# Performance work log

Measured on AMD Instinct MI355X. Metric: run time of the kernel, lower is better.

## Reference

```python
import jax, jax.numpy as jnp
import numpy as np

D_MODEL = 1024
N_HEADS = 16
FACTOR = 2
KEY_DIM = D_MODEL // N_HEADS            # 64
HEAD_DIM = D_MODEL * FACTOR // N_HEADS  # 128
SCALING = KEY_DIM ** -0.5
BSZ, SEQ = 2, 2048


def _rel_pos(slen):
    # angle: 1/10000**linspace(0,1,key_dim//2), each value repeated twice
    half = jnp.asarray(1.0) / jnp.power(10000.0, jnp.linspace(0.0, 1.0, KEY_DIM // 2))
    angle = jnp.repeat(half, 2)                              # [key_dim]
    decay = jnp.log(1.0 - 2.0 ** (-5.0 - jnp.arange(N_HEADS, dtype=jnp.float32)))  # [h], negative
    idx = jnp.arange(slen, dtype=jnp.float32)
    sin = jnp.sin(idx[:, None] * angle[None, :])             # [s, key_dim]
    cos = jnp.cos(idx[:, None] * angle[None, :])
    diff = idx[:, None] - idx[None, :]                       # [s, s]
    tril = diff >= 0
    mask = jnp.where(tril[None], jnp.exp(diff[None] * decay[:, None, None]), 0.0)  # [h, s, s]
    mask = mask / jnp.sqrt(mask.sum(axis=-1, keepdims=True))
    return sin, cos, mask


def _rotate_every_two(x):
    x1 = x[..., ::2]
    x2 = x[..., 1::2]
    return jnp.stack((-x2, x1), axis=-1).reshape(x.shape)


def _theta_shift(x, sin, cos):
    return x * cos + _rotate_every_two(x) * sin


def setup_inputs() -> dict:
    key = jax.random.key(0)
    ks = jax.random.split(key, 11)
    s = 1.0 / np.sqrt(D_MODEL)
    s2 = 1.0 / np.sqrt(D_MODEL * FACTOR)
    return {
        "x": jax.random.normal(ks[0], (BSZ, SEQ, D_MODEL), jnp.float32),
        "q_w": jax.random.uniform(ks[1], (D_MODEL, D_MODEL), jnp.float32, -s, s),
        "q_b": jax.random.uniform(ks[2], (D_MODEL,), jnp.float32, -s, s),
        "k_w": jax.random.uniform(ks[3], (D_MODEL, D_MODEL), jnp.float32, -s, s),
        "k_b": jax.random.uniform(ks[4], (D_MODEL,), jnp.float32, -s, s),
        "v_w": jax.random.uniform(ks[5], (D_MODEL, D_MODEL * FACTOR), jnp.float32, -s, s),
        "v_b": jax.random.uniform(ks[6], (D_MODEL * FACTOR,), jnp.float32, -s, s),
        "g_w": jax.random.uniform(ks[7], (D_MODEL, D_MODEL * FACTOR), jnp.float32, -s, s),
        "g_b": jax.random.uniform(ks[8], (D_MODEL * FACTOR,), jnp.float32, -s, s),
        "o_w": jax.random.uniform(ks[9], (D_MODEL * FACTOR, D_MODEL), jnp.float32, -s2, s2),
        "o_b": jax.random.uniform(ks[10], (D_MODEL,), jnp.float32, -s2, s2),
    }


def _forward(x, q_w, q_b, k_w, k_b, v_w, v_b, g_w, g_b, o_w, o_b):
    bsz, slen, _ = x.shape
    sin, cos, mask = _rel_pos(slen)
    q = x @ q_w + q_b
    k = (x @ k_w + k_b) * SCALING
    v = x @ v_w + v_b
    g = x @ g_w + g_b
    # [b, h, s, key_dim]
    q = q.reshape(bsz, slen, N_HEADS, KEY_DIM).transpose(0, 2, 1, 3)
    k = k.reshape(bsz, slen, N_HEADS, KEY_DIM).transpose(0, 2, 1, 3)
    qr = _theta_shift(q, sin, cos)
    kr = _theta_shift(k, sin, cos)
    vr = v.reshape(bsz, slen, N_HEADS, HEAD_DIM).transpose(0, 2, 1, 3)  # [b,h,s,head_dim]
    qk = jnp.einsum('bhmd,bhnd->bhmn', qr, kr) * mask                  # decay-masked scores
    denom = jnp.clip(jnp.abs(jax.lax.stop_gradient(qk).sum(axis=-1, keepdims=True)), 1.0, None)
    qk = qk / denom
    out = jnp.einsum('bhmn,bhnd->bhmd', qk, vr).transpose(0, 2, 1, 3)  # [b,s,h,head_dim]
    # per-head LayerNorm over head_dim, no affine
    mu = out.mean(axis=-1, keepdims=True)
    var = out.var(axis=-1, keepdims=True)
    out = (out - mu) / jnp.sqrt(var + 1e-5)
    out = out.reshape(bsz, slen, N_HEADS * HEAD_DIM)
    out = jax.nn.silu(g) * out
    return out @ o_w + o_b


def reference(x, q_w, q_b, k_w, k_b, v_w, v_b, g_w, g_b, o_w, o_b):
    return _forward(x, q_w, q_b, k_w, k_b, v_w, v_b, g_w, g_b, o_w, o_b)
```

## Files before the change

### kernel.cpp

```cpp
#include <hip/hip_runtime.h>
#include <hip/hip_bf16.h>


typedef __hip_bfloat16 bf16;
typedef short bf16x4 __attribute__((ext_vector_type(4)));
typedef short bf16x8 __attribute__((ext_vector_type(8)));
typedef float floatx4 __attribute__((ext_vector_type(4)));

#define B_SZ 2
#define SEQ 2048
#define NH 16
#define KD 64
#define HD 128

#define ASYNC16(gp, lp)                                                             \
  __builtin_amdgcn_global_load_lds(                                                 \
      (const __attribute__((address_space(1))) unsigned int*)(unsigned long long)(const void*)(gp), \
      (__attribute__((address_space(3))) unsigned int*)(unsigned int)(unsigned long long)(void*)(lp), \
      16, 0, 0)

__device__ __forceinline__ float b2f(bf16 x) { return __bfloat162float(x); }
__device__ __forceinline__ bf16 f2b(float x) { return __float2bfloat16(x); }

#define MFMA16(a, bb, c) __builtin_amdgcn_mfma_f32_16x16x32_bf16(a, bb, c, 0, 0, 0)

__global__ void convert_k(const float* __restrict__ in, bf16* __restrict__ out) {
  int i = blockIdx.x * 256 + threadIdx.x;
  float4 v = reinterpret_cast<const float4*>(in)[i];
  union { bf16 h[4]; bf16x4 v4; } u;
  u.h[0] = f2b(v.x); u.h[1] = f2b(v.y); u.h[2] = f2b(v.z); u.h[3] = f2b(v.w);
  reinterpret_cast<bf16x4*>(out)[i] = u.v4;
}

__global__ void transpose_k(const float* __restrict__ in, bf16* __restrict__ out,
                            int K, int N) {
  __shared__ float tile[32][33];
  int tx = threadIdx.x, ty = threadIdx.y;
  int n0 = blockIdx.x * 32, k0 = blockIdx.y * 32;
#pragma unroll
  for (int j = 0; j < 4; ++j)
    tile[ty + j * 8][tx] = in[(size_t)(k0 + ty + j * 8) * N + n0 + tx];
  __syncthreads();
#pragma unroll
  for (int j = 0; j < 4; ++j)
    out[(size_t)(n0 + ty + j * 8) * K + k0 + tx] = f2b(tile[tx][ty + j * 8]);
}

template <int BM, int BN, int KDIM, int MODE>
__global__ __launch_bounds__(256, 2) void gemm_bt(
    const bf16* __restrict__ A, const bf16* __restrict__ Bt, int Ndim,
    const float* __restrict__ bias_q, const float* __restrict__ bias_k,
    const float* __restrict__ bias_v, const float* __restrict__ bias_g,
    float* __restrict__ outCqk, bf16* __restrict__ out_v,
    float* __restrict__ out_g, float* __restrict__ outF) {
  __shared__ bf16 As[BM * 32];
  __shared__ bf16 Bs[BN * 32];
  const int tid = threadIdx.x;
  const int wave = tid >> 6, lane = tid & 63;
  const int quad = lane >> 4, l16 = lane & 15;
  const int m0 = blockIdx.y * BM, n0 = blockIdx.x * BN;
  constexpr int FI = BM / 32;
  constexpr int FJ = BN / 32;
  const int wm = (wave >> 1) * (BM / 2), wn = (wave & 1) * (BN / 2);

  floatx4 acc[FI][FJ] = {};

  for (int k0 = 0; k0 < KDIM; k0 += 32) {
#pragma unroll
    for (int j = 0; j < BM / 64; ++j) {
      int cbase = (j * 4 + wave) * 64;
      int c = cbase + lane;
      const bf16* g = A + (size_t)(m0 + (c >> 2)) * KDIM + k0 + (c & 3) * 8;
      ASYNC16(g, &As[cbase * 8]);
    }
#pragma unroll
    for (int j = 0; j < BN / 64; ++j) {
      int cbase = (j * 4 + wave) * 64;
      int c = cbase + lane;
      const bf16* g = Bt + (size_t)(n0 + (c >> 2)) * KDIM + k0 + (c & 3) * 8;
      ASYNC16(g, &Bs[cbase * 8]);
    }
    __syncthreads();

    bf16x8 af[FI], bfr[FJ];
#pragma unroll
    for (int i = 0; i < FI; ++i)
      af[i] = *(const bf16x8*)&As[(wm + i * 16 + l16) * 32 + quad * 8];
#pragma unroll
    for (int j = 0; j < FJ; ++j)
      bfr[j] = *(const bf16x8*)&Bs[(wn + j * 16 + l16) * 32 + quad * 8];
#pragma unroll
    for (int i = 0; i < FI; ++i)
#pragma unroll
      for (int j = 0; j < FJ; ++j)
        acc[i][j] = MFMA16(af[i], bfr[j], acc[i][j]);
    __syncthreads();
  }

#pragma unroll
  for (int i = 0; i < FI; ++i) {
#pragma unroll
    for (int j = 0; j < FJ; ++j) {
      int gn = n0 + wn + j * 16 + l16;
      if (MODE == 0 && gn >= 2048 && gn < 4096) {
        int jj = gn - 2048;
        int s0 = m0 + wm + i * 16 + quad * 4;
        union { bf16 e[4]; unsigned long long u8; } pk;
#pragma unroll
        for (int r = 0; r < 4; ++r) pk.e[r] = f2b(acc[i][j][r] + bias_v[jj]);
        int b2 = s0 >> 11, srel = s0 & 2047;
        int h2 = jj >> 7, dloc = jj & 127;
        size_t bh2 = (size_t)b2 * NH + h2;
        size_t idx = ((bh2 * 64 + (srel >> 5)) * 8 + (dloc >> 4)) * 512 +
                     (size_t)(((srel >> 3) & 3) * 16 + (dloc & 15)) * 8 +
                     (srel & 7);
        *(unsigned long long*)&out_v[idx] = pk.u8;
      } else {
#pragma unroll
        for (int r = 0; r < 4; ++r) {
          int gm = m0 + wm + i * 16 + quad * 4 + r;
          float v = acc[i][j][r];
          if (MODE == 1) {
            v += bias_q[gn];
            outF[(size_t)gm * Ndim + gn] = v;
          } else {
            if (gn < 2048) {
              bool is_k = gn >= 1024;
              int jj = is_k ? gn - 1024 : gn;
              v += is_k ? bias_k[jj] : bias_q[jj];
              if (is_k) v *= 0.125f;
              outCqk[(size_t)gm * 2048 + gn] = v;
            } else {
              int jj = gn - 4096;
              v += bias_g[jj];
              out_g[(size_t)gm * 2048 + jj] = v;
            }
          }
        }
      }
    }
  }
}

__global__ void router_k(const float* __restrict__ Cqk,
                         bf16* __restrict__ qh, bf16* __restrict__ ql,
                         bf16* __restrict__ kh, bf16* __restrict__ kl) {
  int t = blockIdx.x * 256 + threadIdx.x;
  int row = t >> 10, pc = t & 1023;
  int b = row >> 11, s = row & 2047;
  bool is_k = pc >= 512;
  int jj = (pc - (is_k ? 512 : 0)) * 2;
  int h = jj >> 6, d = jj & 63, ii = d >> 1;
  float2 v = *(const float2*)&Cqk[(size_t)row * 2048 + pc * 2];
  float half = exp2f(-(float)ii * (13.287712379549449f / 31.0f));
  float ang = (float)s * half;
  float sn = sinf(ang), cs = cosf(ang);
  float e = v.x * cs - v.y * sn;
  float o = v.y * cs + v.x * sn;
  bf16 eh = f2b(e), oh = f2b(o);
  bf16 el = f2b(e - b2f(eh)), ol = f2b(o - b2f(oh));
  size_t idx = (((size_t)b * NH + h) * SEQ + s) * KD + d;
  bf16* ph = is_k ? kh : qh;
  bf16* pl = is_k ? kl : ql;
  union { bf16 h2[2]; unsigned u; } uh, ul;
  uh.h2[0] = eh; uh.h2[1] = oh;
  ul.h2[0] = el; ul.h2[1] = ol;
  *(unsigned*)&ph[idx] = uh.u;
  *(unsigned*)&pl[idx] = ul.u;
}

__global__ __launch_bounds__(128, 2) void retention_k(
    const bf16* __restrict__ qh, const bf16* __restrict__ ql,
    const bf16* __restrict__ kh, const bf16* __restrict__ kl,
    const bf16* __restrict__ vf, const float* __restrict__ g,
    bf16* __restrict__ gated) {
  __shared__ bf16 KHs[2][32 * 64];
  __shared__ bf16 KLs[2][32 * 64];
  const int tid = threadIdx.x;
  const int wave = tid >> 6, lane = tid & 63;
  const int quad = lane >> 4, l16 = lane & 15;
  const int bid = blockIdx.x;
  const int px_raw = bid & 31;
  const int seg = bid >> 5;
  const int h = seg & 15, b = seg >> 4;
  const int px = ((seg >> 3) & 1) ? (31 - px_raw) : px_raw;
  const int bh = b * NH + h;
  const int bt_h = 63 - px;
  const int bt_l = px;
  const int m0h = bt_h * 32 + wave * 16;
  const int m0l = bt_l * 32 + wave * 16;
  const int ntiles = bt_h + 1;
  const int lt_ntiles = bt_l + 1;

  const float t = exp2f(-(float)(5 + h));
  const float lng = log1pf(-t);
  const float log2g = lng * 1.44269504088896340736f;

  float rfh, rfl;
  {
    int mh = m0h + l16, ml = m0l + l16;
    rfh = exp2f((float)mh * log2g) *
          rsqrtf(-expm1f((float)(mh + 1) * lng) / t);
    rfl = exp2f((float)ml * log2g) *
          rsqrtf(-expm1f((float)(ml + 1) * lng) / t);
  }
  const float gstep = exp2f(-32.0f * log2g);
  float cfq[8];
#pragma unroll
  for (int i = 0; i < 8; ++i) {
    int hh = i >> 2, r = i & 3;
    cfq[i] = exp2f(-(float)(hh * 16 + quad * 4 + r) * log2g);
  }

  const size_t qoffh = ((size_t)bh * SEQ + m0h + l16) * KD;
  const size_t qoffl = ((size_t)bh * SEQ + m0l + l16) * KD;
  bf16x8 aq0h_h = *(const bf16x8*)&qh[qoffh + quad * 8];
  bf16x8 aq1h_h = *(const bf16x8*)&qh[qoffh + 32 + quad * 8];
  bf16x8 aq0l_h = *(const bf16x8*)&ql[qoffh + quad * 8];
  bf16x8 aq1l_h = *(const bf16x8*)&ql[qoffh + 32 + quad * 8];
  bf16x8 aq0h_l = *(const bf16x8*)&qh[qoffl + quad * 8];
  bf16x8 aq1h_l = *(const bf16x8*)&qh[qoffl + 32 + quad * 8];
  bf16x8 aq0l_l = *(const bf16x8*)&ql[qoffl + quad * 8];
  bf16x8 aq1l_l = *(const bf16x8*)&ql[qoffl + 32 + quad * 8];

  floatx4 oacch[8] = {}, oaccl[8] = {};
  float rsh = 0.f, rsl = 0.f;

  const bf16* khb = kh + (size_t)bh * SEQ * KD;
  const bf16* klb = kl + (size_t)bh * SEQ * KD;
  const bf16* vfb = vf + (size_t)bh * 64 * 8 * 512;
  const int lo8 = lane * 8;

  auto stage = [&](int nt, int buf) {
    const int n0s = nt * 32;
#pragma unroll
    for (int j = 0; j < 4; ++j) {
      int cc = wave * 4 + j;
      const bf16* src = (cc < 4) ? khb : klb;
      bf16* dst = (cc < 4) ? KHs[buf] : KLs[buf];
      int r = ((cc & 3) * 8) + (lane >> 3);
      int s = lane & 7;
      int q = (s - r) & 7;
      ASYNC16(src + (size_t)(n0s + r) * KD + q * 8, &dst[(cc & 3) * 512]);
    }
  };

  auto buildPA = [&](const floatx4* sc, float rf, float& rs, int n0,
                     int m0) -> bf16x8 {
    const int m = m0 + l16;
    const bool full = (m0 >= n0 + 31);
    unsigned d[4];
#pragma unroll
    for (int hh = 0; hh < 2; ++hh) {
      float p[4];
#pragma unroll
      for (int r = 0; r < 4; ++r) {
        float pv;
        if (full) {
          pv = sc[hh][r] * rf * cfq[hh * 4 + r];
        } else {
          int n = n0 + hh * 16 + quad * 4 + r;
          pv = (m >= n) ? sc[hh][r] * rf * cfq[hh * 4 + r] : 0.f;
        }
        rs += pv;
        p[r] = pv;
      }
      union { bf16 hx[2]; unsigned u; } u0, u1;
      u0.hx[0] = f2b(p[0]); u0.hx[1] = f2b(p[1]);
      u1.hx[0] = f2b(p[2]); u1.hx[1] = f2b(p[3]);
      d[hh * 2 + 0] = u0.u;
      d[hh * 2 + 1] = u1.u;
    }
    unsigned a0 = d[0], b0 = d[2];
    asm("v_permlane32_swap_b32 %0, %1" : "+v"(a0), "+v"(b0));
    asm("v_permlane16_swap_b32 %0, %1" : "+v"(a0), "+v"(b0));
    unsigned a1 = d[1], b1 = d[3];
    asm("v_permlane32_swap_b32 %0, %1" : "+v"(a1), "+v"(b1));
    asm("v_permlane16_swap_b32 %0, %1" : "+v"(a1), "+v"(b1));
    union { unsigned u[4]; bf16x8 v; } pu;
    pu.u[0] = a0; pu.u[1] = a1; pu.u[2] = b0; pu.u[3] = b1;
    return pu.v;
  };

  stage(0, 0);
  for (int nt = 0; nt < ntiles; ++nt) {
    const int n0 = nt * 32;
    const int cur = nt & 1;
    asm volatile("s_waitcnt vmcnt(0) lgkmcnt(0)" ::: "memory");
    __syncthreads();

    bf16x8 vv[8];
#pragma unroll
    for (int c = 0; c < 8; ++c)
      vv[c] = *(const bf16x8*)(vfb + ((size_t)nt * 8 + c) * 512 + lo8);

    {
      int pf = (nt + 1 < ntiles) ? nt + 1 : nt;
      stage(pf, cur ^ 1);
    }

    const bool hact = (n0 <= m0h + 15);
    const bool lact = (n0 <= m0l + 15);

    floatx4 sch[2], scl[2];
#pragma unroll
    for (int hh = 0; hh < 2; ++hh) {
      int krow = hh * 16 + l16;
      int c0 = ((quad + krow) & 7) * 8;
      int c1 = ((quad + 4 + krow) & 7) * 8;
      bf16x8 bkh0 = *(const bf16x8*)&KHs[cur][krow * 64 + c0];
      bf16x8 bkh1 = *(const bf16x8*)&KHs[cur][krow * 64 + c1];
      bf16x8 bkl0 = *(const bf16x8*)&KLs[cur][krow * 64 + c0];
      bf16x8 bkl1 = *(const bf16x8*)&KLs[cur][krow * 64 + c1];
      if (hact) {
        floatx4 z1 = {0.f, 0.f, 0.f, 0.f}, z2 = z1, z3 = z1;
        z1 = MFMA16(bkh0, aq0h_h, z1);
        z2 = MFMA16(bkh0, aq0l_h, z2);
        z3 = MFMA16(bkl0, aq0h_h, z3);
        z1 = MFMA16(bkh1, aq1h_h, z1);
        z2 = MFMA16(bkh1, aq1l_h, z2);
        z3 = MFMA16(bkl1, aq1h_h, z3);
        sch[hh] = z1 + z2 + z3;
      }
      if (lact) {
        floatx4 z1 = {0.f, 0.f, 0.f, 0.f}, z2 = z1, z3 = z1;
        z1 = MFMA16(bkh0, aq0h_l, z1);
        z2 = MFMA16(bkh0, aq0l_l, z2);
        z3 = MFMA16(bkl0, aq0h_l, z3);
        z1 = MFMA16(bkh1, aq1h_l, z1);
        z2 = MFMA16(bkh1, aq1l_l, z2);
        z3 = MFMA16(bkl1, aq1h_l, z3);
        scl[hh] = z1 + z2 + z3;
      }
    }

    bf16x8 pah, pal;
    if (hact) pah = buildPA(sch, rfh, rsh, n0, m0h);
    if (lact) pal = buildPA(scl, rfl, rsl, n0, m0l);
    rfh *= gstep;
    if (nt + 1 < lt_ntiles) rfl *= gstep;

#pragma unroll
    for (int dt = 0; dt < 8; ++dt) {
      if (hact) oacch[dt] = MFMA16(pah, vv[dt], oacch[dt]);
      if (lact) oaccl[dt] = MFMA16(pal, vv[dt], oaccl[dt]);
    }
  }

  auto finalize = [&](floatx4* oacc, float rowsum, int m0) {
    float v = rowsum;
    v += __shfl_xor(v, 16);
    v += __shfl_xor(v, 32);
    float inv_den[4];
#pragma unroll
    for (int r = 0; r < 4; ++r) {
      float dsum = __shfl(v, quad * 4 + r);
      inv_den[r] = 1.0f / fmaxf(fabsf(dsum), 1.0f);
    }
    float s1[4] = {}, s2[4] = {};
#pragma unroll
    for (int dt = 0; dt < 8; ++dt) {
#pragma unroll
      for (int r = 0; r < 4; ++r) {
        float vv2 = oacc[dt][r] * inv_den[r];
        oacc[dt][r] = vv2;
        s1[r] += vv2;
        s2[r] += vv2 * vv2;
      }
    }
    float mean[4], istd[4];
#pragma unroll
    for (int r = 0; r < 4; ++r) {
      float a = s1[r], q2 = s2[r];
      a += __shfl_xor(a, 1); a += __shfl_xor(a, 2);
      a += __shfl_xor(a, 4); a += __shfl_xor(a, 8);
      q2 += __shfl_xor(q2, 1); q2 += __shfl_xor(q2, 2);
      q2 += __shfl_xor(q2, 4); q2 += __shfl_xor(q2, 8);
      mean[r] = a * (1.0f / 128.0f);
      float var = q2 * (1.0f / 128.0f) - mean[r] * mean[r];
      istd[r] = rsqrtf(fmaxf(var, 0.0f) + 1e-5f);
    }
#pragma unroll
    for (int dt = 0; dt < 8; ++dt) {
#pragma unroll
      for (int r = 0; r < 4; ++r) {
        int m = m0 + quad * 4 + r;
        int col = h * HD + dt * 16 + l16;
        float vv2 = (oacc[dt][r] - mean[r]) * istd[r];
        float gv = g[((size_t)b * SEQ + m) * 2048 + col];
        float sg = gv / (1.0f + expf(-gv));
        gated[((size_t)b * SEQ + m) * 2048 + col] = f2b(sg * vv2);
      }
    }
  };
  finalize(oacch, rsh, m0h);
  finalize(oaccl, rsl, m0l);
}

extern "C" void kernel_launch(void* const* d_in, const int* in_sizes, int n_in,
                              void* d_out, int out_size, void* d_ws,
                              size_t ws_size, hipStream_t stream) {
  const float* x   = (const float*)d_in[0];
  const float* q_w = (const float*)d_in[1];
  const float* q_b = (const float*)d_in[2];
  const float* k_w = (const float*)d_in[3];
  const float* k_b = (const float*)d_in[4];
  const float* v_w = (const float*)d_in[5];
  const float* v_b = (const float*)d_in[6];
  const float* g_w = (const float*)d_in[7];
  const float* g_b = (const float*)d_in[8];
  const float* o_w = (const float*)d_in[9];
  const float* o_b = (const float*)d_in[10];

  char* ws = (char*)d_ws;
  bf16* Wt    = (bf16*)ws; ws += (size_t)6144 * 1024 * 2;
  bf16* oT    = (bf16*)ws; ws += (size_t)1024 * 2048 * 2;
  bf16* xb    = (bf16*)ws; ws += (size_t)4096 * 1024 * 2;
  float* Cqk  = (float*)ws; ws += (size_t)4096 * 2048 * 4;
  bf16* qhb   = (bf16*)ws; ws += (size_t)32 * 2048 * 64 * 2;
  bf16* qlb   = (bf16*)ws; ws += (size_t)32 * 2048 * 64 * 2;
  bf16* khb   = (bf16*)ws; ws += (size_t)32 * 2048 * 64 * 2;
  bf16* klb   = (bf16*)ws; ws += (size_t)32 * 2048 * 64 * 2;
  bf16* vfb   = (bf16*)ws; ws += (size_t)32 * 64 * 8 * 512 * 2;
  float* gbuf = (float*)ws; ws += (size_t)2 * 2048 * 2048 * 4;
  bf16* gated = (bf16*)ws; ws += (size_t)4096 * 2048 * 2;

  convert_k<<<(4096 * 1024 / 4) / 256, 256, 0, stream>>>(x, xb);

  dim3 tb(32, 8);
  transpose_k<<<dim3(1024 / 32, 1024 / 32), tb, 0, stream>>>(q_w, Wt, 1024, 1024);
  transpose_k<<<dim3(1024 / 32, 1024 / 32), tb, 0, stream>>>(k_w, Wt + (size_t)1024 * 1024, 1024, 1024);
  transpose_k<<<dim3(2048 / 32, 1024 / 32), tb, 0, stream>>>(v_w, Wt + (size_t)2048 * 1024, 1024, 2048);
  transpose_k<<<dim3(2048 / 32, 1024 / 32), tb, 0, stream>>>(g_w, Wt + (size_t)4096 * 1024, 1024, 2048);
  transpose_k<<<dim3(1024 / 32, 2048 / 32), tb, 0, stream>>>(o_w, oT, 2048, 1024);

  gemm_bt<128, 128, 1024, 0><<<dim3(6144 / 128, 4096 / 128), 256, 0, stream>>>(
      xb, Wt, 6144, q_b, k_b, v_b, g_b, Cqk, vfb, gbuf, nullptr);

  router_k<<<(4096 * 1024) / 256, 256, 0, stream>>>(Cqk, qhb, qlb, khb, klb);

  retention_k<<<dim3(1024), 128, 0, stream>>>(
      qhb, qlb, khb, klb, vfb, gbuf, gated);

  gemm_bt<128, 64, 2048, 1><<<dim3(1024 / 64, 4096 / 128), 256, 0, stream>>>(
      gated, oT, 1024, o_b, nullptr, nullptr, nullptr, nullptr, nullptr,
      nullptr, (float*)d_out);
}
```

Measured before the change: 333.1 us.

## Restructure retention kernel to 4 waves per contiguous 64-row block

Replaces the paired high/low row-tile scheme (two 32-row tiles per 128-thread block for load balance) with 256-thread blocks where each of four waves owns one 16-row strip of a contiguous 64-row group. The causal loop now runs over 2*grp+2 key tiles, and waves whose strip has no work skip V loads and MFMAs. This halves per-thread accumulator state, which frees registers for higher occupancy. In exchange it loses the per-block triangular load balancing, so block runtimes vary more, and the K staging cost is shared across more waves.

Result: no change. 337.1 us, median of 2 (+1.2%).

```diff
diff --git a/kernel.cpp b/kernel.cpp
--- a/kernel.cpp
+++ b/kernel.cpp
@@ -169,7 +169,7 @@
   *(unsigned*)&pl[idx] = ul.u;
 }
 
-__global__ __launch_bounds__(128, 2) void retention_k(
+__global__ __launch_bounds__(256, 4) void retention_k(
     const bf16* __restrict__ qh, const bf16* __restrict__ ql,
     const bf16* __restrict__ kh, const bf16* __restrict__ kl,
     const bf16* __restrict__ vf, const float* __restrict__ g,
@@ -180,29 +180,23 @@
   const int wave = tid >> 6, lane = tid & 63;
   const int quad = lane >> 4, l16 = lane & 15;
   const int bid = blockIdx.x;
-  const int px_raw = bid & 31;
-  const int seg = bid >> 5;
-  const int h = seg & 15, b = seg >> 4;
-  const int px = ((seg >> 3) & 1) ? (31 - px_raw) : px_raw;
-  const int bh = b * NH + h;
-  const int bt_h = 63 - px;
-  const int bt_l = px;
-  const int m0h = bt_h * 32 + wave * 16;
-  const int m0l = bt_l * 32 + wave * 16;
-  const int ntiles = bt_h + 1;
-  const int lt_ntiles = bt_l + 1;
+  const int grp_raw = bid & 31;
+  const int bh = bid >> 5;
+  const int h = bh & 15, b = bh >> 4;
+  const int grp = ((bh >> 3) & 1) ? (31 - grp_raw) : grp_raw;
+  const int st = grp * 4 + wave;
+  const int m0 = st * 16;
+  const int ntiles = 2 * grp + 2;
 
   const float t = exp2f(-(float)(5 + h));
   const float lng = log1pf(-t);
   const float log2g = lng * 1.44269504088896340736f;
 
-  float rfh, rfl;
+  float rf;
   {
-    int mh = m0h + l16, ml = m0l + l16;
-    rfh = exp2f((float)mh * log2g) *
-          rsqrtf(-expm1f((float)(mh + 1) * lng) / t);
-    rfl = exp2f((float)ml * log2g) *
-          rsqrtf(-expm1f((float)(ml + 1) * lng) / t);
+    int m = m0 + l16;
+    rf = exp2f((float)m * log2g) *
+         rsqrtf(-expm1f((float)(m + 1) * lng) / t);
   }
   const float gstep = exp2f(-32.0f * log2g);
   float cfq[8];
@@ -212,19 +206,14 @@
     cfq[i] = exp2f(-(float)(hh * 16 + quad * 4 + r) * log2g);
   }
 
-  const size_t qoffh = ((size_t)bh * SEQ + m0h + l16) * KD;
-  const size_t qoffl = ((size_t)bh * SEQ + m0l + l16) * KD;
-  bf16x8 aq0h_h = *(const bf16x8*)&qh[qoffh + quad * 8];
-  bf16x8 aq1h_h = *(const bf16x8*)&qh[qoffh + 32 + quad * 8];
-  bf16x8 aq0l_h = *(const bf16x8*)&ql[qoffh + quad * 8];
-  bf16x8 aq1l_h = *(const bf16x8*)&ql[qoffh + 32 + quad * 8];
-  bf16x8 aq0h_l = *(const bf16x8*)&qh[qoffl + quad * 8];
-  bf16x8 aq1h_l = *(const bf16x8*)&qh[qoffl + 32 + quad * 8];
-  bf16x8 aq0l_l = *(const bf16x8*)&ql[qoffl + quad * 8];
-  bf16x8 aq1l_l = *(const bf16x8*)&ql[qoffl + 32 + quad * 8];
-
-  floatx4 oacch[8] = {}, oaccl[8] = {};
-  float rsh = 0.f, rsl = 0.f;
+  const size_t qoff = ((size_t)bh * SEQ + m0 + l16) * KD;
+  bf16x8 aq0h = *(const bf16x8*)&qh[qoff + quad * 8];
+  bf16x8 aq1h = *(const bf16x8*)&qh[qoff + 32 + quad * 8];
+  bf16x8 aq0l = *(const bf16x8*)&ql[qoff + quad * 8];
+  bf16x8 aq1l = *(const bf16x8*)&ql[qoff + 32 + quad * 8];
+
+  floatx4 oacc[8] = {};
+  float rs = 0.f;
 
   const bf16* khb = kh + (size_t)bh * SEQ * KD;
   const bf16* klb = kl + (size_t)bh * SEQ * KD;
@@ -234,8 +223,8 @@
   auto stage = [&](int nt, int buf) {
     const int n0s = nt * 32;
 #pragma unroll
-    for (int j = 0; j < 4; ++j) {
-      int cc = wave * 4 + j;
+    for (int j = 0; j < 2; ++j) {
+      int cc = wave * 2 + j;
       const bf16* src = (cc < 4) ? khb : klb;
       bf16* dst = (cc < 4) ? KHs[buf] : KLs[buf];
       int r = ((cc & 3) * 8) + (lane >> 3);
@@ -245,8 +234,7 @@
     }
   };
 
-  auto buildPA = [&](const floatx4* sc, float rf, float& rs, int n0,
-                     int m0) -> bf16x8 {
+  auto buildPA = [&](const floatx4* sc, int n0) -> bf16x8 {
     const int m = m0 + l16;
     const bool full = (m0 >= n0 + 31);
     unsigned d[4];
@@ -289,66 +277,52 @@
     asm volatile("s_waitcnt vmcnt(0) lgkmcnt(0)" ::: "memory");
     __syncthreads();
 
+    const bool act = (n0 <= m0 + 15);
+
     bf16x8 vv[8];
-#pragma unroll
-    for (int c = 0; c < 8; ++c)
-      vv[c] = *(const bf16x8*)(vfb + ((size_t)nt * 8 + c) * 512 + lo8);
+    if (act) {
+#pragma unroll
+      for (int c = 0; c < 8; ++c)
+        vv[c] = *(const bf16x8*)(vfb + ((size_t)nt * 8 + c) * 512 + lo8);
+    }
 
     {
       int pf = (nt + 1 < ntiles) ? nt + 1 : nt;
       stage(pf, cur ^ 1);
     }
 
-    const bool hact = (n0 <= m0h + 15);
-    const bool lact = (n0 <= m0l + 15);
-
-    floatx4 sch[2], scl[2];
-#pragma unroll
-    for (int hh = 0; hh < 2; ++hh) {
-      int krow = hh * 16 + l16;
-      int c0 = ((quad + krow) & 7) * 8;
-      int c1 = ((quad + 4 + krow) & 7) * 8;
-      bf16x8 bkh0 = *(const bf16x8*)&KHs[cur][krow * 64 + c0];
-      bf16x8 bkh1 = *(const bf16x8*)&KHs[cur][krow * 64 + c1];
-      bf16x8 bkl0 = *(const bf16x8*)&KLs[cur][krow * 64 + c0];
-      bf16x8 bkl1 = *(const bf16x8*)&KLs[cur][krow * 64 + c1];
-      if (hact) {
+    if (act) {
+      floatx4 sc[2];
+#pragma unroll
+      for (int hh = 0; hh < 2; ++hh) {
+        int krow = hh * 16 + l16;
+        int c0 = ((quad + krow) & 7) * 8;
+        int c1 = ((quad + 4 + krow) & 7) * 8;
+        bf16x8 bkh0 = *(const bf16x8*)&KHs[cur][krow * 64 + c0];
+        bf16x8 bkh1 = *(const bf16x8*)&KHs[cur][krow * 64 + c1];
+        bf16x8 bkl0 = *(const bf16x8*)&KLs[cur][krow * 64 + c0];
+        bf16x8 bkl1 = *(const bf16x8*)&KLs[cur][krow * 64 + c1];
         floatx4 z1 = {0.f, 0.f, 0.f, 0.f}, z2 = z1, z3 = z1;
-        z1 = MFMA16(bkh0, aq0h_h, z1);
-        z2 = MFMA16(bkh0, aq0l_h, z2);
-        z3 = MFMA16(bkl0, aq0h_h, z3);
-        z1 = MFMA16(bkh1, aq1h_h, z1);
-        z2 = MFMA16(bkh1, aq1l_h, z2);
-        z3 = MFMA16(bkl1, aq1h_h, z3);
-        sch[hh] = z1 + z2 + z3;
+        z1 = MFMA16(bkh0, aq0h, z1);
+        z2 = MFMA16(bkh0, aq0l, z2);
+        z3 = MFMA16(bkl0, aq0h, z3);
+        z1 = MFMA16(bkh1, aq1h, z1);
+        z2 = MFMA16(bkh1, aq1l, z2);
+        z3 = MFMA16(bkl1, aq1h, z3);
+        sc[hh] = z1 + z2 + z3;
       }
-      if (lact) {
-        floatx4 z1 = {0.f, 0.f, 0.f, 0.f}, z2 = z1, z3 = z1;
-        z1 = MFMA16(bkh0, aq0h_l, z1);
-        z2 = MFMA16(bkh0, aq0l_l, z2);
-        z3 = MFMA16(bkl0, aq0h_l, z3);
-        z1 = MFMA16(bkh1, aq1h_l, z1);
-        z2 = MFMA16(bkh1, aq1l_l, z2);
-        z3 = MFMA16(bkl1, aq1h_l, z3);
-        scl[hh] = z1 + z2 + z3;
-      }
-    }
-
-    bf16x8 pah, pal;
-    if (hact) pah = buildPA(sch, rfh, rsh, n0, m0h);
-    if (lact) pal = buildPA(scl, rfl, rsl, n0, m0l);
-    rfh *= gstep;
-    if (nt + 1 < lt_ntiles) rfl *= gstep;
-
-#pragma unroll
-    for (int dt = 0; dt < 8; ++dt) {
-      if (hact) oacch[dt] = MFMA16(pah, vv[dt], oacch[dt]);
-      if (lact) oaccl[dt] = MFMA16(pal, vv[dt], oaccl[dt]);
-    }
-  }
-
-  auto finalize = [&](floatx4* oacc, float rowsum, int m0) {
-    float v = rowsum;
+
+      bf16x8 pa = buildPA(sc, n0);
+      rf *= gstep;
+
+#pragma unroll
+      for (int dt = 0; dt < 8; ++dt)
+        oacc[dt] = MFMA16(pa, vv[dt], oacc[dt]);
+    }
+  }
+
+  {
+    float v = rs;
     v += __shfl_xor(v, 16);
     v += __shfl_xor(v, 32);
     float inv_den[4];
@@ -392,9 +366,7 @@
         gated[((size_t)b * SEQ + m) * 2048 + col] = f2b(sg * vv2);
       }
     }
-  };
-  finalize(oacch, rsh, m0h);
-  finalize(oaccl, rsl, m0l);
+  }
 }
 
 extern "C" void kernel_launch(void* const* d_in, const int* in_sizes, int n_in,
@@ -439,7 +411,7 @@
 
   router_k<<<(4096 * 1024) / 256, 256, 0, stream>>>(Cqk, qhb, qlb, khb, klb);
 
-  retention_k<<<dim3(1024), 128, 0, stream>>>(
+  retention_k<<<dim3(1024), 256, 0, stream>>>(
       qhb, qlb, khb, klb, vfb, gbuf, gated);
 
   gemm_bt<128, 64, 2048, 1><<<dim3(1024 / 64, 4096 / 128), 256, 0, stream>>>(
```
